# Performance work log

Hardware: AMD Instinct MI355X
Metric: run time of the kernel (lower is better)

The kernel has to match this reference:

```python
import jax, jax.numpy as jnp
import numpy as np

N, D_IN, D_OUT, Q_DIM = 4096, 256, 256, 64


def _xavier(key, shape):
    fan_in, fan_out = shape[-2], shape[-1]
    bound = float(np.sqrt(6.0 / (fan_in + fan_out)))
    return jax.random.uniform(key, shape, jnp.float32, -bound, bound)


def setup_inputs() -> dict:
    key = jax.random.key(0)
    k_x, k_q, k_w, k_b = jax.random.split(key, 4)
    x = jax.random.normal(k_x, (N, D_IN), jnp.float32)
    query_vectors = jax.random.normal(k_q, (N, Q_DIM), jnp.float32)
    W_1 = _xavier(k_w, (Q_DIM, D_IN, D_OUT))  # xavier over last two dims (matches torch on 3D)
    b_1 = _xavier(k_b, (Q_DIM, D_OUT))
    return {"x": x, "query_vectors": query_vectors, "W_1": W_1, "b_1": b_1}


def reference(x, query_vectors, W_1, b_1):
    # Per-sample dynamic weight: W[n] = sum_d q[n,d] * W_1[d]; then x[n] @ W[n] + q[n] @ b_1.
    # Fused single contraction avoids materializing the [n, i, o] tensor; same math.
    out = jnp.einsum('ni,nd,dio->no', x, query_vectors, W_1)
    out = out + query_vectors @ b_1
    return out
```

## Files before the change

### kernel.cpp

```cpp
#include <hip/hip_runtime.h>
#include <stdint.h>


typedef _Float16 f16;
typedef f16 f16x8 __attribute__((ext_vector_type(8)));
typedef float f32x16 __attribute__((ext_vector_type(16)));

#define NROWS 4096
#define QDIM 64

__global__ __launch_bounds__(256) void prep(const float* __restrict__ W,
                                            const float* __restrict__ B1,
                                            f16* __restrict__ Wt) {
  const int b = blockIdx.x, t = threadIdx.x;
  if (b < 512) {
    const int sg = b >> 6, ic = (b >> 3) & 7, dd = b & 7;
    const int g = b + (sg ? 2 : 0);
    const int k0 = ((sg << 3) + dd) * 256 + (ic << 5);
#pragma unroll
    for (int r = 0; r < 4; ++r) {
      const int gidx = (r << 8) + t;
      const int n = gidx & 255, sh = gidx >> 8;
      f16x8 h;
#pragma unroll
      for (int j = 0; j < 8; ++j)
        h[j] = (f16)W[(size_t)(k0 + (sh << 3) + j) * 256 + n];
      *(f16x8*)(Wt + (size_t)g * 8192 + (size_t)gidx * 8) = h;
    }
  } else {
    const int cc = b - 512;
#pragma unroll
    for (int r = 0; r < 4; ++r) {
      const int gidx = (r << 8) + t;
      const int n = gidx & 255, sh = gidx >> 8;
      f16x8 h;
#pragma unroll
      for (int j = 0; j < 8; ++j)
        h[j] = (f16)B1[(size_t)((cc << 5) + (sh << 3) + j) * 256 + n];
      *(f16x8*)(Wt + (size_t)(64 + cc) * 8192 + (size_t)gidx * 8) = h;
    }
  }
}

#define LOADW(D, P)                          \
  do {                                       \
    D[0] = *(const f16x8*)(P);               \
    D[1] = *(const f16x8*)((P) + 512);       \
    D[2] = *(const f16x8*)((P) + 8192);      \
    D[3] = *(const f16x8*)((P) + 8704);      \
  } while (0)

#define XFRAG(DST, PTR)                                                \
  do {                                                                 \
    float4 a_ = *(const float4*)(PTR);                                 \
    float4 b_ = *(const float4*)((PTR) + 4);                           \
    f16x8 h_;                                                          \
    h_[0] = (f16)a_.x; h_[1] = (f16)a_.y; h_[2] = (f16)a_.z;           \
    h_[3] = (f16)a_.w; h_[4] = (f16)b_.x; h_[5] = (f16)b_.y;           \
    h_[6] = (f16)b_.z; h_[7] = (f16)b_.w;                              \
    DST = h_;                                                          \
  } while (0)

#define LOADX_F(D, IC)                                  \
  do {                                                  \
    const float* xb_ = xr0 + ((IC) << 5);               \
    XFRAG(D[0], xb_);                                   \
    XFRAG(D[1], xb_ + 8192);                            \
    XFRAG(D[2], xb_ + 16);                              \
    XFRAG(D[3], xb_ + 8208);                            \
  } while (0)

#define MFMA8(XF, DD, WW)                                                        \
  do {                                                                           \
    const f16 q0_ = qr[0][DD], q1_ = qr[1][DD];                                  \
    f16x8 a00_ = XF[0] * q0_, a10_ = XF[1] * q1_;                                \
    f16x8 a01_ = XF[2] * q0_, a11_ = XF[3] * q1_;                                \
    acc[0][0] = __builtin_amdgcn_mfma_f32_32x32x16_f16(a00_, WW[0], acc[0][0], 0, 0, 0); \
    acc[1][0] = __builtin_amdgcn_mfma_f32_32x32x16_f16(a10_, WW[0], acc[1][0], 0, 0, 0); \
    acc[0][1] = __builtin_amdgcn_mfma_f32_32x32x16_f16(a00_, WW[1], acc[0][1], 0, 0, 0); \
    acc[1][1] = __builtin_amdgcn_mfma_f32_32x32x16_f16(a10_, WW[1], acc[1][1], 0, 0, 0); \
    acc[0][0] = __builtin_amdgcn_mfma_f32_32x32x16_f16(a01_, WW[2], acc[0][0], 0, 0, 0); \
    acc[1][0] = __builtin_amdgcn_mfma_f32_32x32x16_f16(a11_, WW[2], acc[1][0], 0, 0, 0); \
    acc[0][1] = __builtin_amdgcn_mfma_f32_32x32x16_f16(a01_, WW[3], acc[0][1], 0, 0, 0); \
    acc[1][1] = __builtin_amdgcn_mfma_f32_32x32x16_f16(a11_, WW[3], acc[1][1], 0, 0, 0); \
  } while (0)

#define MFMA8Q(QF, WW)                                                           \
  do {                                                                           \
    acc[0][0] = __builtin_amdgcn_mfma_f32_32x32x16_f16(QF[0], WW[0], acc[0][0], 0, 0, 0); \
    acc[1][0] = __builtin_amdgcn_mfma_f32_32x32x16_f16(QF[1], WW[0], acc[1][0], 0, 0, 0); \
    acc[0][1] = __builtin_amdgcn_mfma_f32_32x32x16_f16(QF[0], WW[1], acc[0][1], 0, 0, 0); \
    acc[1][1] = __builtin_amdgcn_mfma_f32_32x32x16_f16(QF[1], WW[1], acc[1][1], 0, 0, 0); \
    acc[0][0] = __builtin_amdgcn_mfma_f32_32x32x16_f16(QF[2], WW[2], acc[0][0], 0, 0, 0); \
    acc[1][0] = __builtin_amdgcn_mfma_f32_32x32x16_f16(QF[3], WW[2], acc[1][0], 0, 0, 0); \
    acc[0][1] = __builtin_amdgcn_mfma_f32_32x32x16_f16(QF[2], WW[3], acc[0][1], 0, 0, 0); \
    acc[1][1] = __builtin_amdgcn_mfma_f32_32x32x16_f16(QF[3], WW[3], acc[1][1], 0, 0, 0); \
  } while (0)

#define STEP(LB, ADDR, XF, DD, UB)   \
  do {                               \
    LOADW(LB, (ADDR));               \
    MFMA8(XF, DD, UB);               \
  } while (0)

__global__ __launch_bounds__(256, 2) void mlp_main(const float* __restrict__ Q,
                                                   const float* __restrict__ X,
                                                   const f16* __restrict__ Wt,
                                                   float* __restrict__ Pp,
                                                   float* __restrict__ out,
                                                   int useP) {
  const int bid = blockIdx.x;
  const int sg = bid & 7;
  const int mb = bid >> 3;
  const int t = threadIdx.x;
  const int w = t >> 6;
  const int l = t & 63;
  const int l31 = l & 31;
  const int hf = l >> 5;

  const char* wg = (const char*)(Wt + (size_t)((sg << 6) + (sg ? 2 : 0)) * 8192);
  const int wl = (hf << 12) + (w << 10) + (l31 << 4);
  const char* wgl = wg + wl;

  const float* xr0 = X + (size_t)((mb << 6) + l31) * 256 + (hf << 3);

  f16 qr[2][8];
#pragma unroll
  for (int mt = 0; mt < 2; ++mt) {
    const float* qp = Q + (size_t)((mb << 6) + (mt << 5) + l31) * QDIM + (sg << 3);
#pragma unroll
    for (int dd = 0; dd < 8; ++dd) qr[mt][dd] = (f16)qp[dd];
  }

  f32x16 acc[2][2];
#pragma unroll
  for (int a = 0; a < 2; ++a)
#pragma unroll
    for (int bq = 0; bq < 2; ++bq)
#pragma unroll
      for (int r = 0; r < 16; ++r) acc[a][bq][r] = 0.f;

  f16x8 Wb0[4], Wb1[4], Wb2[4], Wb3[4], xfA[4], xfB[4];

  const int ic0 = (mb & 3) << 1;

  LOADW(Wb0, wgl + ((size_t)ic0 << 17));
  LOADW(Wb1, wgl + ((size_t)ic0 << 17) + 16384);
  LOADW(Wb2, wgl + ((size_t)ic0 << 17) + 32768);
  LOADX_F(xfA, ic0);

  for (int so = 0; so < 4; ++so) {
    const int icP = (ic0 + (so << 1)) & 7;
    const char* cpb = wgl + ((size_t)icP << 17);
    const char* cpn = (so == 3) ? wgl + ((size_t)64 << 14)
                                : wgl + ((size_t)((icP + 2) & 7) << 17);
    LOADX_F(xfB, icP + 1);
    STEP(Wb3, cpb + (3 << 14),  xfA, 0, Wb0);
    STEP(Wb0, cpb + (4 << 14),  xfA, 1, Wb1);
    STEP(Wb1, cpb + (5 << 14),  xfA, 2, Wb2);
    STEP(Wb2, cpb + (6 << 14),  xfA, 3, Wb3);
    STEP(Wb3, cpb + (7 << 14),  xfA, 4, Wb0);
    STEP(Wb0, cpb + (8 << 14),  xfA, 5, Wb1);
    STEP(Wb1, cpb + (9 << 14),  xfA, 6, Wb2);
    STEP(Wb2, cpb + (10 << 14), xfA, 7, Wb3);
    LOADX_F(xfA, (icP + 2) & 7);
    STEP(Wb3, cpb + (11 << 14), xfB, 0, Wb0);
    STEP(Wb0, cpb + (12 << 14), xfB, 1, Wb1);
    STEP(Wb1, cpb + (13 << 14), xfB, 2, Wb2);
    STEP(Wb2, cpb + (14 << 14), xfB, 3, Wb3);
    STEP(Wb3, cpb + (15 << 14), xfB, 4, Wb0);
    STEP(Wb0, cpn,              xfB, 5, Wb1);
    STEP(Wb1, cpn + (1 << 14),  xfB, 6, Wb2);
    STEP(Wb2, cpn + (2 << 14),  xfB, 7, Wb3);
  }

  if (sg == 0) {
    f16x8 QF0[4], QF1[4];
    const float* qb = Q + (size_t)((mb << 6) + l31) * QDIM + (hf << 3);
    XFRAG(QF0[0], qb);
    XFRAG(QF0[1], qb + 32 * QDIM);
    XFRAG(QF0[2], qb + 16);
    XFRAG(QF0[3], qb + 16 + 32 * QDIM);
    XFRAG(QF1[0], qb + 32);
    XFRAG(QF1[1], qb + 32 + 32 * QDIM);
    XFRAG(QF1[2], qb + 48);
    XFRAG(QF1[3], qb + 48 + 32 * QDIM);
    MFMA8Q(QF0, Wb0);
    MFMA8Q(QF1, Wb1);
  }

  if (useP) {
    float* const ob = Pp + ((size_t)sg << 20);
#pragma unroll
    for (int mt = 0; mt < 2; ++mt)
#pragma unroll
      for (int nt = 0; nt < 2; ++nt)
#pragma unroll
        for (int r = 0; r < 16; ++r) {
          const int row = (mb << 6) + (mt << 5) + (r & 3) + ((r >> 2) << 3) + (hf << 2);
          const int col = (w << 6) + (nt << 5) + l31;
          ob[(size_t)row * 256 + col] = acc[mt][nt][r];
        }
  } else {
#pragma unroll
    for (int mt = 0; mt < 2; ++mt)
#pragma unroll
      for (int nt = 0; nt < 2; ++nt)
#pragma unroll
        for (int r = 0; r < 16; ++r) {
          const int row = (mb << 6) + (mt << 5) + (r & 3) + ((r >> 2) << 3) + (hf << 2);
          const int col = (w << 6) + (nt << 5) + l31;
          atomicAdd(out + (size_t)row * 256 + col, acc[mt][nt][r]);
        }
  }
}

__global__ __launch_bounds__(256) void reduce_k(const float* __restrict__ P,
                                                float* __restrict__ out) {
  const size_t i = (((size_t)blockIdx.x << 8) + threadIdx.x) << 2;
  float4 s = *(const float4*)(P + i);
#pragma unroll
  for (int g = 1; g < 8; ++g) {
    float4 v = *(const float4*)(P + ((size_t)g << 20) + i);
    s.x += v.x; s.y += v.y; s.z += v.z; s.w += v.w;
  }
  *(float4*)(out + i) = s;
}

extern "C" void kernel_launch(void* const* d_in, const int* in_sizes, int n_in,
                              void* d_out, int out_size, void* d_ws, size_t ws_size,
                              hipStream_t stream) {
  (void)in_sizes; (void)n_in; (void)out_size;
  const float* x  = (const float*)d_in[0];
  const float* q  = (const float*)d_in[1];
  const float* W1 = (const float*)d_in[2];
  const float* b1 = (const float*)d_in[3];
  float* out = (float*)d_out;

  const size_t WT_BYTES = (size_t)514 * 16384;
  const size_t NEED = WT_BYTES + ((size_t)8 << 22);
  const int useP = (ws_size >= NEED) ? 1 : 0;
  f16* Wt = (f16*)d_ws;
  float* Pp = (float*)((char*)d_ws + WT_BYTES);

  if (!useP)
    hipMemsetAsync(out, 0, (size_t)NROWS * 256 * sizeof(float), stream);
  prep<<<514, 256, 0, stream>>>(W1, b1, Wt);
  mlp_main<<<512, 256, 0, stream>>>(q, x, Wt, Pp, out, useP);
  if (useP) reduce_k<<<1024, 256, 0, stream>>>(Pp, out);
}
```

Baseline: 136.2 us.

## Use 128-row tiles with 16-way d-split and pre-converted fp16 x

```diff
diff --git a/kernel.cpp b/kernel.cpp
--- a/kernel.cpp
+++ b/kernel.cpp
@@ -8,10 +8,14 @@
 
 #define NROWS 4096
 #define QDIM 64
+#define MBLK 128
+#define SPLIT 16
 
 __global__ __launch_bounds__(256) void prep(const float* __restrict__ W,
                                             const float* __restrict__ B1,
-                                            f16* __restrict__ Wt) {
+                                            const float* __restrict__ X,
+                                            f16* __restrict__ Wt,
+                                            f16* __restrict__ Xt) {
   const int b = blockIdx.x, t = threadIdx.x;
   if (b < 512) {
     const int sg = b >> 6, ic = (b >> 3) & 7, dd = b & 7;
@@ -27,7 +31,7 @@
         h[j] = (f16)W[(size_t)(k0 + (sh << 3) + j) * 256 + n];
       *(f16x8*)(Wt + (size_t)g * 8192 + (size_t)gidx * 8) = h;
     }
-  } else {
+  } else if (b < 514) {
     const int cc = b - 512;
 #pragma unroll
     for (int r = 0; r < 4; ++r) {
@@ -38,6 +42,21 @@
       for (int j = 0; j < 8; ++j)
         h[j] = (f16)B1[(size_t)((cc << 5) + (sh << 3) + j) * 256 + n];
       *(f16x8*)(Wt + (size_t)(64 + cc) * 8192 + (size_t)gidx * 8) = h;
+    }
+  } else {
+    const int idx = b - 514;
+    const int mb = idx >> 2, qtr = idx & 3;
+#pragma unroll
+    for (int r = 0; r < 4; ++r) {
+      const int u = (qtr << 10) + (r << 8) + t;
+      const int row = u & 127, ish = u >> 7;
+      const float* src = X + (size_t)((mb << 7) + row) * 256 + (ish << 3);
+      float4 a = *(const float4*)src;
+      float4 c = *(const float4*)(src + 4);
+      f16x8 h;
+      h[0] = (f16)a.x; h[1] = (f16)a.y; h[2] = (f16)a.z; h[3] = (f16)a.w;
+      h[4] = (f16)c.x; h[5] = (f16)c.y; h[6] = (f16)c.z; h[7] = (f16)c.w;
+      *(f16x8*)(Xt + (size_t)mb * 32768 + (size_t)u * 8) = h;
     }
   }
 }
@@ -50,181 +69,210 @@
     D[3] = *(const f16x8*)((P) + 8704);      \
   } while (0)
 
-#define XFRAG(DST, PTR)                                                \
-  do {                                                                 \
-    float4 a_ = *(const float4*)(PTR);                                 \
-    float4 b_ = *(const float4*)((PTR) + 4);                           \
-    f16x8 h_;                                                          \
-    h_[0] = (f16)a_.x; h_[1] = (f16)a_.y; h_[2] = (f16)a_.z;           \
-    h_[3] = (f16)a_.w; h_[4] = (f16)b_.x; h_[5] = (f16)b_.y;           \
-    h_[6] = (f16)b_.z; h_[7] = (f16)b_.w;                              \
-    DST = h_;                                                          \
-  } while (0)
-
-#define LOADX_F(D, IC)                                  \
-  do {                                                  \
-    const float* xb_ = xr0 + ((IC) << 5);               \
-    XFRAG(D[0], xb_);                                   \
-    XFRAG(D[1], xb_ + 8192);                            \
-    XFRAG(D[2], xb_ + 16);                              \
-    XFRAG(D[3], xb_ + 8208);                            \
-  } while (0)
-
-#define MFMA8(XF, DD, WW)                                                        \
-  do {                                                                           \
-    const f16 q0_ = qr[0][DD], q1_ = qr[1][DD];                                  \
-    f16x8 a00_ = XF[0] * q0_, a10_ = XF[1] * q1_;                                \
-    f16x8 a01_ = XF[2] * q0_, a11_ = XF[3] * q1_;                                \
-    acc[0][0] = __builtin_amdgcn_mfma_f32_32x32x16_f16(a00_, WW[0], acc[0][0], 0, 0, 0); \
-    acc[1][0] = __builtin_amdgcn_mfma_f32_32x32x16_f16(a10_, WW[0], acc[1][0], 0, 0, 0); \
-    acc[0][1] = __builtin_amdgcn_mfma_f32_32x32x16_f16(a00_, WW[1], acc[0][1], 0, 0, 0); \
-    acc[1][1] = __builtin_amdgcn_mfma_f32_32x32x16_f16(a10_, WW[1], acc[1][1], 0, 0, 0); \
-    acc[0][0] = __builtin_amdgcn_mfma_f32_32x32x16_f16(a01_, WW[2], acc[0][0], 0, 0, 0); \
-    acc[1][0] = __builtin_amdgcn_mfma_f32_32x32x16_f16(a11_, WW[2], acc[1][0], 0, 0, 0); \
-    acc[0][1] = __builtin_amdgcn_mfma_f32_32x32x16_f16(a01_, WW[3], acc[0][1], 0, 0, 0); \
-    acc[1][1] = __builtin_amdgcn_mfma_f32_32x32x16_f16(a11_, WW[3], acc[1][1], 0, 0, 0); \
-  } while (0)
-
-#define MFMA8Q(QF, WW)                                                           \
-  do {                                                                           \
-    acc[0][0] = __builtin_amdgcn_mfma_f32_32x32x16_f16(QF[0], WW[0], acc[0][0], 0, 0, 0); \
-    acc[1][0] = __builtin_amdgcn_mfma_f32_32x32x16_f16(QF[1], WW[0], acc[1][0], 0, 0, 0); \
-    acc[0][1] = __builtin_amdgcn_mfma_f32_32x32x16_f16(QF[0], WW[1], acc[0][1], 0, 0, 0); \
-    acc[1][1] = __builtin_amdgcn_mfma_f32_32x32x16_f16(QF[1], WW[1], acc[1][1], 0, 0, 0); \
-    acc[0][0] = __builtin_amdgcn_mfma_f32_32x32x16_f16(QF[2], WW[2], acc[0][0], 0, 0, 0); \
-    acc[1][0] = __builtin_amdgcn_mfma_f32_32x32x16_f16(QF[3], WW[2], acc[1][0], 0, 0, 0); \
-    acc[0][1] = __builtin_amdgcn_mfma_f32_32x32x16_f16(QF[2], WW[3], acc[0][1], 0, 0, 0); \
-    acc[1][1] = __builtin_amdgcn_mfma_f32_32x32x16_f16(QF[3], WW[3], acc[1][1], 0, 0, 0); \
-  } while (0)
-
-#define STEP(LB, ADDR, XF, DD, UB)   \
-  do {                               \
-    LOADW(LB, (ADDR));               \
-    MFMA8(XF, DD, UB);               \
+#define LOADX(D, IC)                                         \
+  do {                                                       \
+    const char* xb_ = xg + ((IC) << 13);                     \
+    _Pragma("unroll")                                        \
+    for (int s_ = 0; s_ < 2; ++s_)                           \
+      _Pragma("unroll")                                      \
+      for (int mt_ = 0; mt_ < 4; ++mt_)                      \
+        D[s_ * 4 + mt_] =                                    \
+            *(const f16x8*)(xb_ + (s_ << 12) + (mt_ << 9));  \
+  } while (0)
+
+#define XFRAG(DST, PTR)                                      \
+  do {                                                       \
+    float4 a_ = *(const float4*)(PTR);                       \
+    float4 b_ = *(const float4*)((PTR) + 4);                 \
+    f16x8 h_;                                                \
+    h_[0] = (f16)a_.x; h_[1] = (f16)a_.y; h_[2] = (f16)a_.z; \
+    h_[3] = (f16)a_.w; h_[4] = (f16)b_.x; h_[5] = (f16)b_.y; \
+    h_[6] = (f16)b_.z; h_[7] = (f16)b_.w;                    \
+    DST = h_;                                                \
+  } while (0)
+
+#define MFMA16(XF, DD, WW)                                                      \
+  do {                                                                          \
+    _Pragma("unroll")                                                           \
+    for (int s_ = 0; s_ < 2; ++s_) {                                            \
+      _Pragma("unroll")                                                         \
+      for (int mt_ = 0; mt_ < 4; ++mt_) {                                       \
+        f16x8 a_ = XF[s_ * 4 + mt_] * qr[mt_][DD];                              \
+        acc[mt_][0] = __builtin_amdgcn_mfma_f32_32x32x16_f16(                   \
+            a_, WW[s_ * 2 + 0], acc[mt_][0], 0, 0, 0);                          \
+        acc[mt_][1] = __builtin_amdgcn_mfma_f32_32x32x16_f16(                   \
+            a_, WW[s_ * 2 + 1], acc[mt_][1], 0, 0, 0);                          \
+      }                                                                         \
+    }                                                                           \
+  } while (0)
+
+#define MFMA16Q(QF, WW)                                                         \
+  do {                                                                          \
+    _Pragma("unroll")                                                           \
+    for (int s_ = 0; s_ < 2; ++s_) {                                            \
+      _Pragma("unroll")                                                         \
+      for (int mt_ = 0; mt_ < 4; ++mt_) {                                       \
+        acc[mt_][0] = __builtin_amdgcn_mfma_f32_32x32x16_f16(                   \
+            QF[s_ * 4 + mt_], WW[s_ * 2 + 0], acc[mt_][0], 0, 0, 0);            \
+        acc[mt_][1] = __builtin_amdgcn_mfma_f32_32x32x16_f16(                   \
+            QF[s_ * 4 + mt_], WW[s_ * 2 + 1], acc[mt_][1], 0, 0, 0);            \
+      }                                                                         \
+    }                                                                           \
   } while (0)
 
 __global__ __launch_bounds__(256, 2) void mlp_main(const float* __restrict__ Q,
-                                                   const float* __restrict__ X,
                                                    const f16* __restrict__ Wt,
-                                                   float* __restrict__ Pp,
+                                                   const f16* __restrict__ Xt,
+                                                   void* __restrict__ Pp,
                                                    float* __restrict__ out,
-                                                   int useP) {
+                                                   int mode) {
   const int bid = blockIdx.x;
-  const int sg = bid & 7;
-  const int mb = bid >> 3;
+  const int sg16 = bid & 15;
+  const int mb = bid >> 4;
   const int t = threadIdx.x;
   const int w = t >> 6;
   const int l = t & 63;
   const int l31 = l & 31;
   const int hf = l >> 5;
 
-  const char* wg = (const char*)(Wt + (size_t)((sg << 6) + (sg ? 2 : 0)) * 8192);
+  const int sg8 = sg16 >> 1;
+  const int dd8b = (sg16 & 1) << 2;
   const int wl = (hf << 12) + (w << 10) + (l31 << 4);
-  const char* wgl = wg + wl;
-
-  const float* xr0 = X + (size_t)((mb << 6) + l31) * 256 + (hf << 3);
-
-  f16 qr[2][8];
-#pragma unroll
-  for (int mt = 0; mt < 2; ++mt) {
-    const float* qp = Q + (size_t)((mb << 6) + (mt << 5) + l31) * QDIM + (sg << 3);
-#pragma unroll
-    for (int dd = 0; dd < 8; ++dd) qr[mt][dd] = (f16)qp[dd];
-  }
-
-  f32x16 acc[2][2];
-#pragma unroll
-  for (int a = 0; a < 2; ++a)
+  const char* wrow = (const char*)Wt +
+      (((size_t)(sg8 * 64 + (sg8 ? 2 : 0) + dd8b)) << 14) + wl;
+
+  const char* xg = (const char*)Xt + ((size_t)mb << 16) + (hf << 11) + (l31 << 4);
+
+  f16 qr[4][4];
+#pragma unroll
+  for (int mt = 0; mt < 4; ++mt) {
+    float4 qv = *(const float4*)(Q + (size_t)((mb << 7) + (mt << 5) + l31) * QDIM +
+                                 (sg16 << 2));
+    qr[mt][0] = (f16)qv.x; qr[mt][1] = (f16)qv.y;
+    qr[mt][2] = (f16)qv.z; qr[mt][3] = (f16)qv.w;
+  }
+
+  f32x16 acc[4][2];
+#pragma unroll
+  for (int a = 0; a < 4; ++a)
 #pragma unroll
     for (int bq = 0; bq < 2; ++bq)
 #pragma unroll
       for (int r = 0; r < 16; ++r) acc[a][bq][r] = 0.f;
 
-  f16x8 Wb0[4], Wb1[4], Wb2[4], Wb3[4], xfA[4], xfB[4];
+  f16x8 WA[4], WB[4], xfA[8], xfB[8];
 
   const int ic0 = (mb & 3) << 1;
 
-  LOADW(Wb0, wgl + ((size_t)ic0 << 17));
-  LOADW(Wb1, wgl + ((size_t)ic0 << 17) + 16384);
-  LOADW(Wb2, wgl + ((size_t)ic0 << 17) + 32768);
-  LOADX_F(xfA, ic0);
+  LOADW(WA, wrow + ((size_t)ic0 << 17));
+  LOADX(xfA, ic0);
 
   for (int so = 0; so < 4; ++so) {
-    const int icP = (ic0 + (so << 1)) & 7;
-    const char* cpb = wgl + ((size_t)icP << 17);
-    const char* cpn = (so == 3) ? wgl + ((size_t)64 << 14)
-                                : wgl + ((size_t)((icP + 2) & 7) << 17);
-    LOADX_F(xfB, icP + 1);
-    STEP(Wb3, cpb + (3 << 14),  xfA, 0, Wb0);
-    STEP(Wb0, cpb + (4 << 14),  xfA, 1, Wb1);
-    STEP(Wb1, cpb + (5 << 14),  xfA, 2, Wb2);
-    STEP(Wb2, cpb + (6 << 14),  xfA, 3, Wb3);
-    STEP(Wb3, cpb + (7 << 14),  xfA, 4, Wb0);
-    STEP(Wb0, cpb + (8 << 14),  xfA, 5, Wb1);
-    STEP(Wb1, cpb + (9 << 14),  xfA, 6, Wb2);
-    STEP(Wb2, cpb + (10 << 14), xfA, 7, Wb3);
-    LOADX_F(xfA, (icP + 2) & 7);
-    STEP(Wb3, cpb + (11 << 14), xfB, 0, Wb0);
-    STEP(Wb0, cpb + (12 << 14), xfB, 1, Wb1);
-    STEP(Wb1, cpb + (13 << 14), xfB, 2, Wb2);
-    STEP(Wb2, cpb + (14 << 14), xfB, 3, Wb3);
-    STEP(Wb3, cpb + (15 << 14), xfB, 4, Wb0);
-    STEP(Wb0, cpn,              xfB, 5, Wb1);
-    STEP(Wb1, cpn + (1 << 14),  xfB, 6, Wb2);
-    STEP(Wb2, cpn + (2 << 14),  xfB, 7, Wb3);
-  }
-
-  if (sg == 0) {
-    f16x8 QF0[4], QF1[4];
-    const float* qb = Q + (size_t)((mb << 6) + l31) * QDIM + (hf << 3);
-    XFRAG(QF0[0], qb);
-    XFRAG(QF0[1], qb + 32 * QDIM);
-    XFRAG(QF0[2], qb + 16);
-    XFRAG(QF0[3], qb + 16 + 32 * QDIM);
-    XFRAG(QF1[0], qb + 32);
-    XFRAG(QF1[1], qb + 32 + 32 * QDIM);
-    XFRAG(QF1[2], qb + 48);
-    XFRAG(QF1[3], qb + 48 + 32 * QDIM);
-    MFMA8Q(QF0, Wb0);
-    MFMA8Q(QF1, Wb1);
-  }
-
-  if (useP) {
-    float* const ob = Pp + ((size_t)sg << 20);
-#pragma unroll
-    for (int mt = 0; mt < 2; ++mt)
+    const int icE = (ic0 + (so << 1)) & 7;
+    const int icO = icE + 1;
+    const char* pe = wrow + ((size_t)icE << 17);
+    const char* po = wrow + ((size_t)icO << 17);
+    const char* pn = (so == 3)
+                         ? ((sg16 == 0) ? (const char*)Wt + ((size_t)64 << 14) + wl : pe)
+                         : wrow + ((size_t)((icE + 2) & 7) << 17);
+    LOADX(xfB, icO);
+    LOADW(WB, pe + 16384);  MFMA16(xfA, 0, WA);
+    LOADW(WA, pe + 32768);  MFMA16(xfA, 1, WB);
+    LOADW(WB, pe + 49152);  MFMA16(xfA, 2, WA);
+    LOADW(WA, po);          MFMA16(xfA, 3, WB);
+    LOADX(xfA, (icE + 2) & 7);
+    LOADW(WB, po + 16384);  MFMA16(xfB, 0, WA);
+    LOADW(WA, po + 32768);  MFMA16(xfB, 1, WB);
+    LOADW(WB, po + 49152);  MFMA16(xfB, 2, WA);
+    LOADW(WA, pn);          MFMA16(xfB, 3, WB);
+  }
+
+  if (sg16 == 0) {
+    const char* b65 = (const char*)Wt + ((size_t)65 << 14) + wl;
+    LOADW(WB, b65);
+    f16x8 QF[8];
+#pragma unroll
+    for (int s = 0; s < 2; ++s)
+#pragma unroll
+      for (int mt = 0; mt < 4; ++mt)
+        XFRAG(QF[s * 4 + mt],
+              Q + (size_t)((mb << 7) + (mt << 5) + l31) * QDIM + (s << 4) + (hf << 3));
+    MFMA16Q(QF, WA);
+#pragma unroll
+    for (int s = 0; s < 2; ++s)
+#pragma unroll
+      for (int mt = 0; mt < 4; ++mt)
+        XFRAG(QF[s * 4 + mt],
+              Q + (size_t)((mb << 7) + (mt << 5) + l31) * QDIM + 32 + (s << 4) + (hf << 3));
+    MFMA16Q(QF, WB);
+  }
+
+  if (mode == 2) {
+    float* P = (float*)Pp + ((size_t)sg16 << 20);
+#pragma unroll
+    for (int mt = 0; mt < 4; ++mt)
 #pragma unroll
       for (int nt = 0; nt < 2; ++nt)
 #pragma unroll
         for (int r = 0; r < 16; ++r) {
-          const int row = (mb << 6) + (mt << 5) + (r & 3) + ((r >> 2) << 3) + (hf << 2);
+          const int row = (mb << 7) + (mt << 5) + (r & 3) + ((r >> 2) << 3) + (hf << 2);
           const int col = (w << 6) + (nt << 5) + l31;
-          ob[(size_t)row * 256 + col] = acc[mt][nt][r];
+          P[(size_t)row * 256 + col] = acc[mt][nt][r];
+        }
+  } else if (mode == 1) {
+    f16* P = (f16*)Pp + ((size_t)sg16 << 20);
+#pragma unroll
+    for (int mt = 0; mt < 4; ++mt)
+#pragma unroll
+      for (int nt = 0; nt < 2; ++nt)
+#pragma unroll
+        for (int r = 0; r < 16; ++r) {
+          const int row = (mb << 7) + (mt << 5) + (r & 3) + ((r >> 2) << 3) + (hf << 2);
+          const int col = (w << 6) + (nt << 5) + l31;
+          P[(size_t)row * 256 + col] = (f16)acc[mt][nt][r];
         }
   } else {
 #pragma unroll
-    for (int mt = 0; mt < 2; ++mt)
+    for (int mt = 0; mt < 4; ++mt)
 #pragma unroll
       for (int nt = 0; nt < 2; ++nt)
 #pragma unroll
         for (int r = 0; r < 16; ++r) {
-          const int row = (mb << 6) + (mt << 5) + (r & 3) + ((r >> 2) << 3) + (hf << 2);
+          const int row = (mb << 7) + (mt << 5) + (r & 3) + ((r >> 2) << 3) + (hf << 2);
           const int col = (w << 6) + (nt << 5) + l31;
           atomicAdd(out + (size_t)row * 256 + col, acc[mt][nt][r]);
         }
   }
 }
 
-__global__ __launch_bounds__(256) void reduce_k(const float* __restrict__ P,
+__global__ __launch_bounds__(256) void reduce32(const float* __restrict__ P,
                                                 float* __restrict__ out) {
   const size_t i = (((size_t)blockIdx.x << 8) + threadIdx.x) << 2;
   float4 s = *(const float4*)(P + i);
 #pragma unroll
-  for (int g = 1; g < 8; ++g) {
+  for (int g = 1; g < 16; ++g) {
     float4 v = *(const float4*)(P + ((size_t)g << 20) + i);
     s.x += v.x; s.y += v.y; s.z += v.z; s.w += v.w;
   }
   *(float4*)(out + i) = s;
+}
+
+__global__ __launch_bounds__(256) void reduce16(const f16* __restrict__ P,
+                                                float* __restrict__ out) {
+  const size_t i8 = ((size_t)blockIdx.x << 8) + threadIdx.x;
+  float s[8];
+#pragma unroll
+  for (int j = 0; j < 8; ++j) s[j] = 0.f;
+#pragma unroll
+  for (int g = 0; g < 16; ++g) {
+    f16x8 v = *(const f16x8*)(P + ((size_t)g << 20) + (i8 << 3));
+#pragma unroll
+    for (int j = 0; j < 8; ++j) s[j] += (float)v[j];
+  }
+  float4 o0 = {s[0], s[1], s[2], s[3]};
+  float4 o1 = {s[4], s[5], s[6], s[7]};
+  *(float4*)(out + (i8 << 3)) = o0;
+  *(float4*)(out + (i8 << 3) + 4) = o1;
 }
 
 extern "C" void kernel_launch(void* const* d_in, const int* in_sizes, int n_in,
@@ -238,14 +286,23 @@
   float* out = (float*)d_out;
 
   const size_t WT_BYTES = (size_t)514 * 16384;
-  const size_t NEED = WT_BYTES + ((size_t)8 << 22);
-  const int useP = (ws_size >= NEED) ? 1 : 0;
+  const size_t XT_BYTES = (size_t)2 * 1024 * 1024;
+  const size_t P32_BYTES = (size_t)16 << 22;
+  const size_t P16_BYTES = (size_t)16 << 21;
+
   f16* Wt = (f16*)d_ws;
-  float* Pp = (float*)((char*)d_ws + WT_BYTES);
-
-  if (!useP)
+  f16* Xt = (f16*)((char*)d_ws + WT_BYTES);
+  void* Pp = (void*)((char*)d_ws + WT_BYTES + XT_BYTES);
+
+  int mode;
+  if (ws_size >= WT_BYTES + XT_BYTES + P32_BYTES) mode = 2;
+  else if (ws_size >= WT_BYTES + XT_BYTES + P16_BYTES) mode = 1;
+  else mode = 0;
+
+  if (mode == 0)
     hipMemsetAsync(out, 0, (size_t)NROWS * 256 * sizeof(float), stream);
-  prep<<<514, 256, 0, stream>>>(W1, b1, Wt);
-  mlp_main<<<512, 256, 0, stream>>>(q, x, Wt, Pp, out, useP);
-  if (useP) reduce_k<<<1024, 256, 0, stream>>>(Pp, out);
-}
+  prep<<<642, 256, 0, stream>>>(W1, b1, x, Wt, Xt);
+  mlp_main<<<512, 256, 0, stream>>>(q, Wt, Xt, Pp, out, mode);
+  if (mode == 2)      reduce32<<<1024, 256, 0, stream>>>((const float*)Pp, out);
+  else if (mode == 1) reduce16<<<512, 256, 0, stream>>>((const f16*)Pp, out);
+}
```

Result: faster. 129.1 us (-5.2%).
